# Performance work log

Hardware: AMD Instinct MI355X
Metric: run time of the kernel (lower is better)

The kernel has to match this reference:

```python
import jax, jax.numpy as jnp
import numpy as np


def setup_inputs() -> dict:
    key = jax.random.key(0)
    kq, kk, kv = jax.random.split(key, 3)
    B, H, S, D = 2, 16, 2048, 128
    Q = jax.random.normal(kq, (B, H, S, D), dtype=jnp.float32)
    K = jax.random.normal(kk, (B, H, S, D), dtype=jnp.float32)
    V = jax.random.normal(kv, (B, H, S, D), dtype=jnp.float32)
    return {"Q": Q, "K": K, "V": V}


def reference(Q, K, V):
    # Unscaled, unmasked attention: softmax(Q K^T) V
    score = jnp.einsum('bhqd,bhkd->bhqk', Q, K)  # [B,H,S,S]
    attn = jax.nn.softmax(score, axis=-1)
    context = jnp.einsum('bhqk,bhkd->bhqd', attn, V)  # [B,H,S,D]
    return context
```

## Files before the change

kernel.cpp:

```cpp
#include <hip/hip_runtime.h>
#include <stdint.h>

#define BH_N 32
#define S_N  2048
#define D_N  128
#define BK   64
#define NT   (S_N / BK)
#define QW   32
#define BQ   128

#define LOG2E 1.4426950408889634f

typedef __bf16    bf16x8 __attribute__((ext_vector_type(8)));
typedef _Float16  f16x8  __attribute__((ext_vector_type(8)));
typedef float     f32x4  __attribute__((ext_vector_type(4)));

union FragU { uint4 u4; uint32_t u[4]; bf16x8 b; };
union FragH { uint4 u4; uint32_t u[4]; f16x8 h; _Float16 e[8]; };

__device__ __forceinline__ uint32_t pack_bf16(float lo, float hi) {
  uint32_t ul = __float_as_uint(lo) + 0x8000u;
  uint32_t uh = __float_as_uint(hi) + 0x8000u;
  return __builtin_amdgcn_perm(uh, ul, 0x07060302u);
}

__device__ __forceinline__ void gl_lds16(const uint16_t* g, uint16_t* l) {
  __builtin_amdgcn_global_load_lds(
      (const __attribute__((address_space(1))) uint32_t*)g,
      (__attribute__((address_space(3))) uint32_t*)l, 16, 0, 0);
}

__global__ __launch_bounds__(256) void prep_kernel(const float* __restrict__ Kg,
                                                   uint16_t* __restrict__ Ko,
                                                   const float* __restrict__ Vg,
                                                   uint16_t* __restrict__ Vtg) {
  if (blockIdx.x < 4096) {
    const int idx = blockIdx.x * 256 + threadIdx.x;
    const int rg = idx >> 4;
    const int g = idx & 15;
    const float* src = Kg + (size_t)idx * 8;
    float4 a = *(const float4*)(src);
    float4 b = *(const float4*)(src + 4);
    FragH w;
    w.e[0] = (_Float16)a.x; w.e[1] = (_Float16)a.y;
    w.e[2] = (_Float16)a.z; w.e[3] = (_Float16)a.w;
    w.e[4] = (_Float16)b.x; w.e[5] = (_Float16)b.y;
    w.e[6] = (_Float16)b.z; w.e[7] = (_Float16)b.w;
    *(uint4*)(Ko + (size_t)rg * 128 + ((g ^ (rg & 7)) * 8)) = w.u4;
    return;
  }
  __shared__ float stg[64][65];
  const int bid = blockIdx.x - 4096;
  const int dt = bid & 1;
  const int st = (bid >> 1) & 31;
  const int bh = bid >> 6;
  const int tid = threadIdx.x;
  {
    const int r = tid >> 4;
    const int c = (tid & 15) * 4;
    const float* Vb = Vg + ((size_t)bh * S_N + (size_t)st * 64) * D_N + dt * 64;
#pragma unroll
    for (int i = 0; i < 4; ++i) {
      float4 x = *(const float4*)(Vb + (size_t)(r + i * 16) * D_N + c);
      stg[r + i * 16][c + 0] = x.x;
      stg[r + i * 16][c + 1] = x.y;
      stg[r + i * 16][c + 2] = x.z;
      stg[r + i * 16][c + 3] = x.w;
    }
  }
  __syncthreads();
  uint16_t* Vo = Vtg + ((size_t)(bh * 32 + st) * 128 + dt * 64) * 64;
  const int gp = tid & 7;
  const int k0 = (gp & 4) * 8 + (gp & 3) * 4;
#pragma unroll
  for (int it = 0; it < 2; ++it) {
    const int drl = it * 32 + (tid >> 3);
    const int d = dt * 64 + drl;
    uint4 w;
    w.x = pack_bf16(stg[k0 + 0][drl], stg[k0 + 1][drl]);
    w.y = pack_bf16(stg[k0 + 2][drl], stg[k0 + 3][drl]);
    w.z = pack_bf16(stg[k0 + 16][drl], stg[k0 + 17][drl]);
    w.w = pack_bf16(stg[k0 + 18][drl], stg[k0 + 19][drl]);
    *(uint4*)(Vo + (size_t)drl * 64 + ((gp ^ (d & 7)) * 8)) = w;
  }
}

__global__ __launch_bounds__(256, 2)
void attn_kernel(const float* __restrict__ Qg, const uint16_t* __restrict__ Kimg,
                 const uint16_t* __restrict__ Vimg, float* __restrict__ Og) {
  __shared__ uint16_t k_lds[2][BK * 128];
  __shared__ uint16_t vt_lds[2][D_N * 64];

  const int tid = threadIdx.x;
  const int bid = blockIdx.x;
  const int bh = bid & 31;
  const int qb = bid >> 5;
  const int wave = tid >> 6;
  const int lane = tid & 63;
  const int l15 = lane & 15;
  const int quad = lane >> 4;
  const int sw = l15 & 7;

  const float*    Qb = Qg + (size_t)bh * S_N * D_N;
  float*          Ob = Og + (size_t)bh * S_N * D_N;
  const uint16_t* Kt0 = Kimg + (size_t)bh * 32 * 64 * 128;
  const uint16_t* Vt0 = Vimg + (size_t)bh * 32 * 128 * 64;

  const int q0 = qb * BQ + wave * QW;
  const int phase = ((qb << 1) | (bh & 1)) & 31;

  FragH qh[2][4];
#pragma unroll
  for (int g = 0; g < 2; ++g) {
    const float* qrow = Qb + (size_t)(q0 + g * 16 + l15) * D_N + quad * 8;
#pragma unroll
    for (int kc = 0; kc < 4; ++kc) {
      float4 x0 = *(const float4*)(qrow + kc * 32);
      float4 x1 = *(const float4*)(qrow + kc * 32 + 4);
      qh[g][kc].e[0] = (_Float16)(x0.x * LOG2E);
      qh[g][kc].e[1] = (_Float16)(x0.y * LOG2E);
      qh[g][kc].e[2] = (_Float16)(x0.z * LOG2E);
      qh[g][kc].e[3] = (_Float16)(x0.w * LOG2E);
      qh[g][kc].e[4] = (_Float16)(x1.x * LOG2E);
      qh[g][kc].e[5] = (_Float16)(x1.y * LOG2E);
      qh[g][kc].e[6] = (_Float16)(x1.z * LOG2E);
      qh[g][kc].e[7] = (_Float16)(x1.w * LOG2E);
    }
  }

  f32x4 oacc[2][8];
  const f32x4 zf = {0.f, 0.f, 0.f, 0.f};
#pragma unroll
  for (int g = 0; g < 2; ++g)
#pragma unroll
    for (int mt = 0; mt < 8; ++mt) oacc[g][mt] = zf;
  float lsum[2] = {0.f, 0.f};

  const int lel = lane * 8;
  auto stage = [&](int ktp, int buf) {
    const uint16_t* ks = Kt0 + (size_t)ktp * (64 * 128);
    const uint16_t* vs = Vt0 + (size_t)ktp * (128 * 64);
    uint16_t* kl = &k_lds[buf][0];
    uint16_t* vl = &vt_lds[buf][0];
#pragma unroll
    for (int i = 0; i < 4; ++i) {
      const int off = (wave * 16 + i * 4) * 128;
      gl_lds16(ks + off + lel, kl + off + lel);
    }
#pragma unroll
    for (int i = 0; i < 4; ++i) {
      const int off = (wave * 32 + i * 8) * 64;
      gl_lds16(vs + off + lel, vl + off + lel);
    }
  };

  stage(phase, 0);
  asm volatile("s_waitcnt vmcnt(0)" ::: "memory");
  __syncthreads();

  for (int kt = 0; kt < NT; ++kt) {
    const int cur = kt & 1;
    if (kt + 1 < NT) stage((kt + 1 + phase) & 31, cur ^ 1);

    const uint16_t* kl = &k_lds[cur][0];
    const uint16_t* vl = &vt_lds[cur][0];

    f32x4 sacc[2][4];
#pragma unroll
    for (int kc = 0; kc < 4; ++kc) {
#pragma unroll
      for (int mt = 0; mt < 4; ++mt) {
        FragH a;
        a.u4 = *(const uint4*)(kl + (mt * 16 + l15) * 128 + (((kc * 4 + quad) ^ sw) * 8));
#pragma unroll
        for (int g = 0; g < 2; ++g) {
          f32x4 c = (kc == 0) ? zf : sacc[g][mt];
          sacc[g][mt] = __builtin_amdgcn_mfma_f32_16x16x32_f16(a.h, qh[g][kc].h, c, 0, 0, 0);
        }
      }
    }

#pragma unroll
    for (int half = 0; half < 2; ++half) {
      FragU bq[2];
#pragma unroll
      for (int g = 0; g < 2; ++g) {
        const f32x4 s0 = sacc[g][half * 2 + 0];
        const f32x4 s1 = sacc[g][half * 2 + 1];
        float a0 = __builtin_amdgcn_exp2f(s0.x);
        float a1 = __builtin_amdgcn_exp2f(s0.y);
        float a2 = __builtin_amdgcn_exp2f(s0.z);
        float a3 = __builtin_amdgcn_exp2f(s0.w);
        float b0 = __builtin_amdgcn_exp2f(s1.x);
        float b1 = __builtin_amdgcn_exp2f(s1.y);
        float b2 = __builtin_amdgcn_exp2f(s1.z);
        float b3 = __builtin_amdgcn_exp2f(s1.w);
        lsum[g] += ((a0 + a1) + (a2 + a3)) + ((b0 + b1) + (b2 + b3));
        bq[g].u[0] = pack_bf16(a0, a1);
        bq[g].u[1] = pack_bf16(a2, a3);
        bq[g].u[2] = pack_bf16(b0, b1);
        bq[g].u[3] = pack_bf16(b2, b3);
      }
#pragma unroll
      for (int mt = 0; mt < 8; ++mt) {
        FragU a;
        a.u4 = *(const uint4*)(vl + (mt * 16 + l15) * 64 + (((half * 4 + quad) ^ sw) * 8));
#pragma unroll
        for (int g = 0; g < 2; ++g) {
          oacc[g][mt] = __builtin_amdgcn_mfma_f32_16x16x32_bf16(a.b, bq[g].b, oacc[g][mt], 0, 0, 0);
        }
      }
    }

    asm volatile("s_waitcnt vmcnt(0)" ::: "memory");
    __syncthreads();
  }

#pragma unroll
  for (int g = 0; g < 2; ++g) {
    float l = lsum[g];
    l += __shfl_xor(l, 16);
    l += __shfl_xor(l, 32);
    const float rl = 1.0f / l;
#pragma unroll
    for (int mt = 0; mt < 8; ++mt) {
      float4 w;
      w.x = oacc[g][mt].x * rl;
      w.y = oacc[g][mt].y * rl;
      w.z = oacc[g][mt].z * rl;
      w.w = oacc[g][mt].w * rl;
      *(float4*)(Ob + (size_t)(q0 + g * 16 + l15) * D_N + mt * 16 + quad * 4) = w;
    }
  }
}

extern "C" void kernel_launch(void* const* d_in, const int* in_sizes, int n_in,
                              void* d_out, int out_size, void* d_ws, size_t ws_size,
                              hipStream_t stream) {
  const float* Q = (const float*)d_in[0];
  const float* K = (const float*)d_in[1];
  const float* V = (const float*)d_in[2];
  float* O = (float*)d_out;

  const size_t half = (size_t)BH_N * S_N * D_N * sizeof(uint16_t);
  if (ws_size < 2 * half) return;
  uint16_t* Vt = (uint16_t*)d_ws;
  uint16_t* Kh = (uint16_t*)((char*)d_ws + half);

  prep_kernel<<<dim3(4096 + BH_N * 32 * 2), dim3(256), 0, stream>>>(K, Kh, V, Vt);
  attn_kernel<<<dim3(S_N / BQ * BH_N), dim3(256), 0, stream>>>(Q, Kh, Vt, O);
}
```

Measured before the change: 205.6 us.

## Software-pipeline QK^T of next tile with softmax/PV of current tile

Restructures the main loop so that the QK^T MFMAs for tile t+1 are issued between the exp/pack of tile t and its PV MFMAs, using ping-pong score accumulators and a manually unrolled loop of two iterations. K is prefetched two tiles ahead and V one tile ahead, with separate staging. s_setprio is raised around the MFMA blocks so the matrix work gets issue priority over other waves' VALU work. The intent is to hide the exp/VALU latency behind matrix work; the cost is more live registers, which risks spills or lower occupancy under launch_bounds(256,2).

```diff
diff --git a/kernel.cpp b/kernel.cpp
--- a/kernel.cpp
+++ b/kernel.cpp
@@ -85,6 +85,101 @@
   }
 }
 
+#define STAGE_K(ktp, buf) do {                                                  \
+    const uint16_t* ks_ = Kt0 + (size_t)(ktp) * (64 * 128);                     \
+    uint16_t* kl_ = &k_lds[buf][0];                                             \
+    _Pragma("unroll")                                                           \
+    for (int i_ = 0; i_ < 4; ++i_) {                                            \
+      const int off_ = (wave * 16 + i_ * 4) * 128;                              \
+      gl_lds16(ks_ + off_ + lel, kl_ + off_ + lel);                             \
+    }                                                                           \
+  } while (0)
+
+#define STAGE_V(ktp, buf) do {                                                  \
+    const uint16_t* vs_ = Vt0 + (size_t)(ktp) * (128 * 64);                     \
+    uint16_t* vl_ = &vt_lds[buf][0];                                            \
+    _Pragma("unroll")                                                           \
+    for (int i_ = 0; i_ < 4; ++i_) {                                            \
+      const int off_ = (wave * 32 + i_ * 8) * 64;                               \
+      gl_lds16(vs_ + off_ + lel, vl_ + off_ + lel);                             \
+    }                                                                           \
+  } while (0)
+
+#define QK_PHASE(kbuf, SACC) do {                                               \
+    const uint16_t* kl_ = &k_lds[kbuf][0];                                      \
+    __builtin_amdgcn_s_setprio(1);                                              \
+    _Pragma("unroll")                                                           \
+    for (int kc_ = 0; kc_ < 4; ++kc_) {                                         \
+      _Pragma("unroll")                                                         \
+      for (int mt_ = 0; mt_ < 4; ++mt_) {                                       \
+        FragH a_;                                                               \
+        a_.u4 = *(const uint4*)(kl_ + (mt_ * 16 + l15) * 128 +                  \
+                                (((kc_ * 4 + quad) ^ sw) * 8));                 \
+        _Pragma("unroll")                                                       \
+        for (int g_ = 0; g_ < 2; ++g_) {                                        \
+          f32x4 c_ = (kc_ == 0) ? zf : SACC[g_][mt_];                           \
+          SACC[g_][mt_] = __builtin_amdgcn_mfma_f32_16x16x32_f16(               \
+              a_.h, qh[g_][kc_].h, c_, 0, 0, 0);                                \
+        }                                                                       \
+      }                                                                         \
+    }                                                                           \
+    __builtin_amdgcn_s_setprio(0);                                              \
+  } while (0)
+
+#define BODY(T, SIN, SOUT) do {                                                 \
+    const int t_ = (T);                                                         \
+    if (t_ + 2 < NT) STAGE_K((t_ + 2 + phase) & 31, t_ & 1);                    \
+    if (t_ + 1 < NT) STAGE_V((t_ + 1 + phase) & 31, (t_ + 1) & 1);              \
+            \
+    FragU bq_[2][2];                                                            \
+    _Pragma("unroll")                                                           \
+    for (int h_ = 0; h_ < 2; ++h_) {                                            \
+      _Pragma("unroll")                                                         \
+      for (int g_ = 0; g_ < 2; ++g_) {                                          \
+        const f32x4 s0_ = SIN[g_][h_ * 2 + 0];                                  \
+        const f32x4 s1_ = SIN[g_][h_ * 2 + 1];                                  \
+        float a0_ = __builtin_amdgcn_exp2f(s0_.x);                              \
+        float a1_ = __builtin_amdgcn_exp2f(s0_.y);                              \
+        float a2_ = __builtin_amdgcn_exp2f(s0_.z);                              \
+        float a3_ = __builtin_amdgcn_exp2f(s0_.w);                              \
+        float b0_ = __builtin_amdgcn_exp2f(s1_.x);                              \
+        float b1_ = __builtin_amdgcn_exp2f(s1_.y);                              \
+        float b2_ = __builtin_amdgcn_exp2f(s1_.z);                              \
+        float b3_ = __builtin_amdgcn_exp2f(s1_.w);                              \
+        lsum[g_] += ((a0_ + a1_) + (a2_ + a3_)) + ((b0_ + b1_) + (b2_ + b3_));  \
+        bq_[h_][g_].u[0] = pack_bf16(a0_, a1_);                                 \
+        bq_[h_][g_].u[1] = pack_bf16(a2_, a3_);                                 \
+        bq_[h_][g_].u[2] = pack_bf16(b0_, b1_);                                 \
+        bq_[h_][g_].u[3] = pack_bf16(b2_, b3_);                                 \
+      }                                                                         \
+    }                                                                           \
+                        \
+    if (t_ + 1 < NT) QK_PHASE((t_ + 1) & 1, SOUT);                              \
+                         \
+    {                                                                           \
+      const uint16_t* vl_ = &vt_lds[t_ & 1][0];                                 \
+      _Pragma("unroll")                                                         \
+      for (int h_ = 0; h_ < 2; ++h_) {                                          \
+        FragU vf_[8];                                                           \
+        _Pragma("unroll")                                                       \
+        for (int mt_ = 0; mt_ < 8; ++mt_)                                       \
+          vf_[mt_].u4 = *(const uint4*)(vl_ + (mt_ * 16 + l15) * 64 +           \
+                                        (((h_ * 4 + quad) ^ sw) * 8));          \
+        __builtin_amdgcn_s_setprio(1);                                          \
+        _Pragma("unroll")                                                       \
+        for (int mt_ = 0; mt_ < 8; ++mt_) {                                     \
+          _Pragma("unroll")                                                     \
+          for (int g_ = 0; g_ < 2; ++g_)                                        \
+            oacc[g_][mt_] = __builtin_amdgcn_mfma_f32_16x16x32_bf16(            \
+                vf_[mt_].b, bq_[h_][g_].b, oacc[g_][mt_], 0, 0, 0);             \
+        }                                                                       \
+        __builtin_amdgcn_s_setprio(0);                                          \
+      }                                                                         \
+    }                                                                           \
+    asm volatile("s_waitcnt vmcnt(0)" ::: "memory");                            \
+    __syncthreads();                                                            \
+  } while (0)
+
 __global__ __launch_bounds__(256, 2)
 void attn_kernel(const float* __restrict__ Qg, const uint16_t* __restrict__ Kimg,
                  const uint16_t* __restrict__ Vimg, float* __restrict__ Og) {
@@ -108,6 +203,7 @@
 
   const int q0 = qb * BQ + wave * QW;
   const int phase = ((qb << 1) | (bh & 1)) & 31;
+  const int lel = lane * 8;
 
   FragH qh[2][4];
 #pragma unroll
@@ -136,84 +232,20 @@
     for (int mt = 0; mt < 8; ++mt) oacc[g][mt] = zf;
   float lsum[2] = {0.f, 0.f};
 
-  const int lel = lane * 8;
-  auto stage = [&](int ktp, int buf) {
-    const uint16_t* ks = Kt0 + (size_t)ktp * (64 * 128);
-    const uint16_t* vs = Vt0 + (size_t)ktp * (128 * 64);
-    uint16_t* kl = &k_lds[buf][0];
-    uint16_t* vl = &vt_lds[buf][0];
-#pragma unroll
-    for (int i = 0; i < 4; ++i) {
-      const int off = (wave * 16 + i * 4) * 128;
-      gl_lds16(ks + off + lel, kl + off + lel);
-    }
-#pragma unroll
-    for (int i = 0; i < 4; ++i) {
-      const int off = (wave * 32 + i * 8) * 64;
-      gl_lds16(vs + off + lel, vl + off + lel);
-    }
-  };
-
-  stage(phase, 0);
+  f32x4 saccA[2][4];
+  f32x4 saccB[2][4];
+
+  STAGE_K(phase, 0);
+  STAGE_V(phase, 0);
+  STAGE_K((1 + phase) & 31, 1);
   asm volatile("s_waitcnt vmcnt(0)" ::: "memory");
   __syncthreads();
-
-  for (int kt = 0; kt < NT; ++kt) {
-    const int cur = kt & 1;
-    if (kt + 1 < NT) stage((kt + 1 + phase) & 31, cur ^ 1);
-
-    const uint16_t* kl = &k_lds[cur][0];
-    const uint16_t* vl = &vt_lds[cur][0];
-
-    f32x4 sacc[2][4];
-#pragma unroll
-    for (int kc = 0; kc < 4; ++kc) {
-#pragma unroll
-      for (int mt = 0; mt < 4; ++mt) {
-        FragH a;
-        a.u4 = *(const uint4*)(kl + (mt * 16 + l15) * 128 + (((kc * 4 + quad) ^ sw) * 8));
-#pragma unroll
-        for (int g = 0; g < 2; ++g) {
-          f32x4 c = (kc == 0) ? zf : sacc[g][mt];
-          sacc[g][mt] = __builtin_amdgcn_mfma_f32_16x16x32_f16(a.h, qh[g][kc].h, c, 0, 0, 0);
-        }
-      }
-    }
-
-#pragma unroll
-    for (int half = 0; half < 2; ++half) {
-      FragU bq[2];
-#pragma unroll
-      for (int g = 0; g < 2; ++g) {
-        const f32x4 s0 = sacc[g][half * 2 + 0];
-        const f32x4 s1 = sacc[g][half * 2 + 1];
-        float a0 = __builtin_amdgcn_exp2f(s0.x);
-        float a1 = __builtin_amdgcn_exp2f(s0.y);
-        float a2 = __builtin_amdgcn_exp2f(s0.z);
-        float a3 = __builtin_amdgcn_exp2f(s0.w);
-        float b0 = __builtin_amdgcn_exp2f(s1.x);
-        float b1 = __builtin_amdgcn_exp2f(s1.y);
-        float b2 = __builtin_amdgcn_exp2f(s1.z);
-        float b3 = __builtin_amdgcn_exp2f(s1.w);
-        lsum[g] += ((a0 + a1) + (a2 + a3)) + ((b0 + b1) + (b2 + b3));
-        bq[g].u[0] = pack_bf16(a0, a1);
-        bq[g].u[1] = pack_bf16(a2, a3);
-        bq[g].u[2] = pack_bf16(b0, b1);
-        bq[g].u[3] = pack_bf16(b2, b3);
-      }
-#pragma unroll
-      for (int mt = 0; mt < 8; ++mt) {
-        FragU a;
-        a.u4 = *(const uint4*)(vl + (mt * 16 + l15) * 64 + (((half * 4 + quad) ^ sw) * 8));
-#pragma unroll
-        for (int g = 0; g < 2; ++g) {
-          oacc[g][mt] = __builtin_amdgcn_mfma_f32_16x16x32_bf16(a.b, bq[g].b, oacc[g][mt], 0, 0, 0);
-        }
-      }
-    }
-
-    asm volatile("s_waitcnt vmcnt(0)" ::: "memory");
-    __syncthreads();
+  QK_PHASE(0, saccA);
+  __syncthreads();
+
+  for (int t2 = 0; t2 < NT; t2 += 2) {
+    BODY(t2 + 0, saccA, saccB);
+    BODY(t2 + 1, saccB, saccA);
   }
 
 #pragma unroll
```

Result: slower. 217.2 us (+5.6%).
